# Optimization experiments

Measured on AMD Instinct MI355X. Metric: run time of the kernel, lower is better.

Reference implementation:

```python
import jax, jax.numpy as jnp
import numpy as np

I = 256   # input_size
H = 512   # hidden_size
B = 8192  # batch


def setup_inputs() -> dict:
    key = jax.random.key(0)
    ks = jax.random.split(key, 16)
    def rn(k, shape, scale):
        return (jax.random.normal(k, shape, dtype=jnp.float32) * scale)
    inp = {
        "x": rn(ks[0], (B, I), 1.0),
        "h": rn(ks[1], (B, H), 0.1),
        "c": rn(ks[2], (B, H), 0.1),
        # attention MLP: Linear(I+H -> I), Linear(I -> I)
        "aw0": rn(ks[3], (I, I + H), (I + H) ** -0.5),
        "ab0": rn(ks[4], (I,), 0.01),
        "aw1": rn(ks[5], (I, I), I ** -0.5),
        "ab1": rn(ks[6], (I,), 0.01),
        # LSTMCell params, PyTorch layout: [4H, I] / [4H, H], gate order i,f,g,o
        "w_ih": rn(ks[7], (4 * H, I), I ** -0.5),
        "b_ih": rn(ks[8], (4 * H,), 0.01),
        "w_hh": rn(ks[9], (4 * H, H), H ** -0.5),
        "b_hh": rn(ks[10], (4 * H,), 0.01),
        # output head: Linear(H -> H), Linear(H -> 1)
        "ow0": rn(ks[11], (H, H), H ** -0.5),
        "ob0": rn(ks[12], (H,), 0.01),
        "ow1": rn(ks[13], (1, H), H ** -0.5),
        "ob1": rn(ks[14], (1,), 0.01),
    }
    return inp


def reference(x, h, c, aw0, ab0, aw1, ab1, w_ih, b_ih, w_hh, b_hh, ow0, ob0, ow1, ob1):
    # attention gate over the input features
    xh = jnp.concatenate([x, h], axis=1)                    # [B, I+H]
    a0 = jax.nn.relu(xh @ aw0.T + ab0)                      # [B, I]
    logits = a0 @ aw1.T + ab1                               # [B, I]
    attn = jax.nn.softmax(logits, axis=1)                   # attention == 1
    x_att = x * attn                                        # [B, I]

    # LSTMCell (torch gate order: i, f, g, o)
    gates = x_att @ w_ih.T + b_ih + h @ w_hh.T + b_hh       # [B, 4H]
    i_g, f_g, g_g, o_g = jnp.split(gates, 4, axis=1)
    i_g = jax.nn.sigmoid(i_g)
    f_g = jax.nn.sigmoid(f_g)
    g_g = jnp.tanh(g_g)
    o_g = jax.nn.sigmoid(o_g)
    c_new = f_g * c + i_g * g_g
    h_new = o_g * jnp.tanh(c_new)

    # 2-layer MLP head -> sigmoid scalar per row
    out = jax.nn.relu(h_new @ ow0.T + ob0)                  # [B, H]
    out = jax.nn.sigmoid(out @ ow1.T + ob1)                 # [B, 1]
    return (out, h_new, c_new, attn)
```

## Files before the change

### kernel.cpp

```cpp
#include <hip/hip_runtime.h>
#include <hip/hip_bf16.h>

#define BROWS 8192
#define IDIM 256
#define HDIM 512
#define KCAT 768
#define G4 2048

typedef __bf16 bf16_t;
typedef bf16_t bf16x8 __attribute__((ext_vector_type(8)));
typedef float f32x4 __attribute__((ext_vector_type(4)));

__device__ __forceinline__ f32x4 mfma16(bf16x8 a, bf16x8 b, f32x4 c) {
    return __builtin_amdgcn_mfma_f32_16x16x32_bf16(a, b, c, 0, 0, 0);
}

__device__ __forceinline__ ushort f2bf(float f) {
    union { float f; unsigned u; } v; v.f = f;
    unsigned u = v.u;
    unsigned r = (u + 0x7fffu + ((u >> 16) & 1u)) >> 16;
    return (ushort)r;
}

__device__ __forceinline__ float bf2f(ushort u) {
    union { unsigned u; float f; } v; v.u = (unsigned)u << 16; return v.f;
}

__device__ __forceinline__ float sigmoidf_(float x) {
    return 1.f / (1.f + __expf(-x));
}
__device__ __forceinline__ float tanhf_(float x) {
    return 1.f - 2.f / (__expf(2.f * x) + 1.f);
}

typedef __attribute__((address_space(1))) const unsigned gas_u32;
typedef __attribute__((address_space(3))) unsigned las_u32;
__device__ __forceinline__ void gld_lds16(const void* g, void* l) {
    __builtin_amdgcn_global_load_lds((gas_u32*)g, (las_u32*)l, 16, 0, 0);
}

__global__ void __launch_bounds__(256) prep_kernel(
        const float* __restrict__ x, const float* __restrict__ h,
        const float* __restrict__ aw0, const float* __restrict__ aw1,
        const float* __restrict__ w_ih, const float* __restrict__ w_hh,
        const float* __restrict__ ow0,
        ushort* __restrict__ xh, ushort* __restrict__ baw0,
        ushort* __restrict__ baw1, ushort* __restrict__ wcat,
        ushort* __restrict__ bow0) {
    int idx = (blockIdx.x * 256 + threadIdx.x) * 4;
    const int N_XH = BROWS * KCAT;
    const int N_AW0 = IDIM * KCAT;
    const int N_AW1 = IDIM * IDIM;
    const int N_WCAT = G4 * KCAT;
    const int N_OW0 = HDIM * HDIM;
    float4 v;
    ushort* dst;
    if (idx < N_XH) {
        int b = idx / KCAT, k = idx - b * KCAT;
        v = (k < IDIM) ? *(const float4*)&x[b * IDIM + k]
                       : *(const float4*)&h[b * HDIM + (k - IDIM)];
        dst = &xh[idx];
    } else if ((idx -= N_XH) < N_AW0) {
        v = *(const float4*)&aw0[idx]; dst = &baw0[idx];
    } else if ((idx -= N_AW0) < N_AW1) {
        v = *(const float4*)&aw1[idx]; dst = &baw1[idx];
    } else if ((idx -= N_AW1) < N_WCAT) {
        int o = idx / KCAT, k = idx - o * KCAT;
        v = (k < IDIM) ? *(const float4*)&w_ih[o * IDIM + k]
                       : *(const float4*)&w_hh[o * HDIM + (k - IDIM)];
        dst = &wcat[idx];
    } else if ((idx -= N_WCAT) < N_OW0) {
        v = *(const float4*)&ow0[idx]; dst = &bow0[idx];
    } else {
        return;
    }
    ushort4 o4 = { f2bf(v.x), f2bf(v.y), f2bf(v.z), f2bf(v.w) };
    *(ushort4*)dst = o4;
}

template<int RELU_BF16, int NFRAG>
__global__ void __launch_bounds__(256) staged_gemm(
        const ushort* __restrict__ A, const ushort* __restrict__ W,
        const float* __restrict__ bias, void* __restrict__ outp,
        int Kdim, int out_ld) {
    __shared__ ushort As[2][4096];
    __shared__ ushort Ws[2][NFRAG * 1024];
    const int tid = threadIdx.x;
    const int lane = tid & 63, wave = tid >> 6;
    const int wm = wave >> 1, wn = wave & 1;
    const int r = lane & 15, g = lane >> 4;
    const int rb = blockIdx.x & 63, cb = blockIdx.x >> 6;
    const int row0 = rb * 128, col0 = cb * (NFRAG * 32);
    const int s_row = tid >> 2;
    const int s_sw = ((tid & 3) ^ ((s_row >> 1) & 3)) * 8;

    const ushort* aBase = A + (size_t)(row0 + s_row) * Kdim + s_sw;
    const ushort* wBase = W + (size_t)(col0 + s_row) * Kdim + s_sw;
    const int step64 = 64 * Kdim;
    const int rsw = (g ^ ((r >> 1) & 3)) * 8;

    f32x4 acc[4][NFRAG] = {};

    auto stage = [&](int buf, int t) {
        const int o = t * 32;
        gld_lds16(aBase + o,          &As[buf][wave * 512]);
        gld_lds16(aBase + o + step64, &As[buf][2048 + wave * 512]);
        gld_lds16(wBase + o,          &Ws[buf][wave * 512]);
        if (NFRAG == 4)
            gld_lds16(wBase + o + step64, &Ws[buf][2048 + wave * 512]);
    };
    auto compute = [&](int buf) {
        bf16x8 af[4], wf[NFRAG];
#pragma unroll
        for (int t = 0; t < 4; t++)
            af[t] = *(const bf16x8*)&As[buf][(wm * 4 + t) * 512 + r * 32 + rsw];
#pragma unroll
        for (int t = 0; t < NFRAG; t++)
            wf[t] = *(const bf16x8*)&Ws[buf][(wn * NFRAG + t) * 512 + r * 32 + rsw];
#pragma unroll
        for (int m = 0; m < 4; m++)
#pragma unroll
            for (int n = 0; n < NFRAG; n++)
                acc[m][n] = mfma16(af[m], wf[n], acc[m][n]);
    };

    stage(0, 0);
    const int NT = Kdim >> 5;
    int cur = 0;
    for (int t = 0; t < NT; t++) {
        __builtin_amdgcn_s_barrier();
        if (t + 1 < NT) {
            stage(cur ^ 1, t + 1);
            if (NFRAG == 4) asm volatile("s_waitcnt vmcnt(4)" ::: "memory");
            else            asm volatile("s_waitcnt vmcnt(3)" ::: "memory");
        } else {
            asm volatile("s_waitcnt vmcnt(0)" ::: "memory");
        }
        __builtin_amdgcn_s_barrier();
        compute(cur);
        cur ^= 1;
    }

#pragma unroll
    for (int n = 0; n < NFRAG; n++) {
        int col = col0 + wn * (NFRAG * 16) + n * 16 + r;
        float bv = bias[col];
#pragma unroll
        for (int m = 0; m < 4; m++) {
            int rbase = row0 + wm * 64 + m * 16 + g * 4;
#pragma unroll
            for (int reg = 0; reg < 4; reg++) {
                float v = acc[m][n][reg] + bv;
                if (RELU_BF16) {
                    v = v > 0.f ? v : 0.f;
                    ((ushort*)outp)[(size_t)(rbase + reg) * out_ld + col] = f2bf(v);
                } else {
                    ((float*)outp)[(size_t)(rbase + reg) * out_ld + col] = v;
                }
            }
        }
    }
}

__global__ void __launch_bounds__(256) attn_softmax(
        const float* __restrict__ logits, const float* __restrict__ x,
        float* __restrict__ attn_out, ushort* __restrict__ xh) {
    const int wave = threadIdx.x >> 6, lane = threadIdx.x & 63;
    const int row = blockIdx.x * 4 + wave;
    float v[4];
    float m = -1e30f;
#pragma unroll
    for (int i = 0; i < 4; i++) {
        v[i] = logits[row * IDIM + i * 64 + lane];
        m = fmaxf(m, v[i]);
    }
#pragma unroll
    for (int s = 32; s; s >>= 1) m = fmaxf(m, __shfl_xor(m, s, 64));
    float sum = 0.f;
#pragma unroll
    for (int i = 0; i < 4; i++) { v[i] = __expf(v[i] - m); sum += v[i]; }
#pragma unroll
    for (int s = 32; s; s >>= 1) sum += __shfl_xor(sum, s, 64);
    float inv = 1.f / sum;
#pragma unroll
    for (int i = 0; i < 4; i++) {
        int idx = i * 64 + lane;
        float a = v[i] * inv;
        attn_out[row * IDIM + idx] = a;
        xh[row * KCAT + idx] = f2bf(x[row * IDIM + idx] * a);
    }
}

__global__ void __launch_bounds__(1024, 4) gates_staged(
        const ushort* __restrict__ A, const ushort* __restrict__ W,
        const float* __restrict__ b_ih, const float* __restrict__ b_hh,
        const float* __restrict__ c_in,
        float* __restrict__ h_out, float* __restrict__ c_out,
        ushort* __restrict__ h_bf) {
    __shared__ ushort As[2 * 8192];
    __shared__ ushort Ws[2 * 8192];
    const int tid = threadIdx.x;
    const int lane = tid & 63, wave = tid >> 6;
    const int wm = wave >> 2, wn = wave & 3;
    const int r = lane & 15, g = lane >> 4;
    const int bid = blockIdx.x;
    const int xcd = bid & 7, local = bid >> 3;
    const int rb = xcd * 4 + (local & 3);
    const int cb = local >> 2;
    const int row0 = rb * 256;
    const int j0 = cb * 64;
    const int rl = lane >> 2, chq = lane & 3;
    const int s_sw = (chq ^ ((rl >> 1) & 3)) * 8;
    const int rsw = (g ^ ((r >> 1) & 3)) * 8;

    auto wrow = [&](int cc) {
        return ((cc >> 4) & 3) * HDIM + j0 + (cc & 15) + ((cc >> 6) << 4);
    };
    const ushort* aP = A + (size_t)(row0 + wave * 16 + rl) * KCAT + s_sw;
    const ushort* wP = W + (size_t)wrow(wave * 16 + rl) * KCAT + s_sw;

    f32x4 acc[4][4] = {};

    auto stage = [&](int buf, int t) {
        const int o = t * 32;
        gld_lds16(aP + o, &As[buf * 8192 + wave * 512]);
        gld_lds16(wP + o, &Ws[buf * 8192 + wave * 512]);
    };
    auto compute = [&](int buf) {
        bf16x8 af[4], wf[4];
#pragma unroll
        for (int m = 0; m < 4; m++)
            af[m] = *(const bf16x8*)&As[buf * 8192 + (wm * 4 + m) * 512 + r * 32 + rsw];
#pragma unroll
        for (int n = 0; n < 4; n++)
            wf[n] = *(const bf16x8*)&Ws[buf * 8192 + (wn * 4 + n) * 512 + r * 32 + rsw];
#pragma unroll
        for (int m = 0; m < 4; m++)
#pragma unroll
            for (int n = 0; n < 4; n++)
                acc[m][n] = mfma16(af[m], wf[n], acc[m][n]);
    };

    stage(0, 0);
    const int NT = KCAT >> 5;
    int cur = 0;
    for (int t = 0; t < NT; t++) {
        __builtin_amdgcn_s_barrier();
        if (t + 1 < NT) {
            stage(cur ^ 1, t + 1);
            asm volatile("s_waitcnt vmcnt(2)" ::: "memory");
        } else {
            asm volatile("s_waitcnt vmcnt(0)" ::: "memory");
        }
        __builtin_amdgcn_s_barrier();
        compute(cur);
        cur ^= 1;
    }

    const int j = j0 + wn * 16 + r;
    float bb[4];
#pragma unroll
    for (int n = 0; n < 4; n++) bb[n] = b_ih[n * HDIM + j] + b_hh[n * HDIM + j];
#pragma unroll
    for (int m = 0; m < 4; m++) {
        int rbase = row0 + wm * 64 + m * 16 + g * 4;
#pragma unroll
        for (int reg = 0; reg < 4; reg++) {
            int row = rbase + reg;
            float ig = sigmoidf_(acc[m][0][reg] + bb[0]);
            float fg = sigmoidf_(acc[m][1][reg] + bb[1]);
            float gg = tanhf_(acc[m][2][reg] + bb[2]);
            float og = sigmoidf_(acc[m][3][reg] + bb[3]);
            float cn = fg * c_in[(size_t)row * HDIM + j] + ig * gg;
            float hn = og * tanhf_(cn);
            c_out[(size_t)row * HDIM + j] = cn;
            h_out[(size_t)row * HDIM + j] = hn;
            h_bf[(size_t)row * HDIM + j] = f2bf(hn);
        }
    }
}

__global__ void __launch_bounds__(256) head_gemv(
        const ushort* __restrict__ Hrelu, const float* __restrict__ ow1,
        const float* __restrict__ ob1, float* __restrict__ outp) {
    const int wave = threadIdx.x >> 6, lane = threadIdx.x & 63;
    const int row = blockIdx.x * 4 + wave;
    typedef ushort u16x8 __attribute__((ext_vector_type(8)));
    u16x8 hv = *(const u16x8*)&Hrelu[(size_t)row * HDIM + lane * 8];
    float4 w0 = *(const float4*)&ow1[lane * 8];
    float4 w1 = *(const float4*)&ow1[lane * 8 + 4];
    float s = bf2f(hv[0]) * w0.x + bf2f(hv[1]) * w0.y + bf2f(hv[2]) * w0.z +
              bf2f(hv[3]) * w0.w + bf2f(hv[4]) * w1.x + bf2f(hv[5]) * w1.y +
              bf2f(hv[6]) * w1.z + bf2f(hv[7]) * w1.w;
#pragma unroll
    for (int sh = 32; sh; sh >>= 1) s += __shfl_xor(s, sh, 64);
    if (lane == 0) outp[row] = 1.f / (1.f + __expf(-(s + ob1[0])));
}

extern "C" void kernel_launch(void* const* d_in, const int* in_sizes, int n_in,
                              void* d_out, int out_size, void* d_ws, size_t ws_size,
                              hipStream_t stream) {
    const float* x    = (const float*)d_in[0];
    const float* h    = (const float*)d_in[1];
    const float* c    = (const float*)d_in[2];
    const float* aw0  = (const float*)d_in[3];
    const float* ab0  = (const float*)d_in[4];
    const float* aw1  = (const float*)d_in[5];
    const float* ab1  = (const float*)d_in[6];
    const float* w_ih = (const float*)d_in[7];
    const float* b_ih = (const float*)d_in[8];
    const float* w_hh = (const float*)d_in[9];
    const float* b_hh = (const float*)d_in[10];
    const float* ow0  = (const float*)d_in[11];
    const float* ob0  = (const float*)d_in[12];
    const float* ow1  = (const float*)d_in[13];
    const float* ob1  = (const float*)d_in[14];

    char* ws = (char*)d_ws;
    ushort* xh     = (ushort*)(ws + 0);
    ushort* a0     = (ushort*)(ws + 12582912);
    float*  logits = (float*) (ws + 16777216);
    ushort* hrelu  = (ushort*)(ws + 16777216);
    ushort* hbf    = (ushort*)(ws + 25165824);
    ushort* baw0   = (ushort*)(ws + 33554432);
    ushort* baw1   = (ushort*)(ws + 33947648);
    ushort* wcat   = (ushort*)(ws + 34078720);
    ushort* bow0   = (ushort*)(ws + 37224448);

    float* outv    = (float*)d_out;
    float* h_out   = outv + 8192;
    float* c_out   = outv + 4202496;
    float* attn_o  = outv + 8396800;

    prep_kernel<<<8192, 256, 0, stream>>>(x, h, aw0, aw1, w_ih, w_hh, ow0,
                                          xh, baw0, baw1, wcat, bow0);
    staged_gemm<1, 2><<<256, 256, 0, stream>>>(xh, baw0, ab0, a0, KCAT, IDIM);
    staged_gemm<0, 2><<<256, 256, 0, stream>>>(a0, baw1, ab1, logits, IDIM, IDIM);
    attn_softmax<<<2048, 256, 0, stream>>>(logits, x, attn_o, xh);
    gates_staged<<<256, 1024, 0, stream>>>(xh, wcat, b_ih, b_hh, c,
                                           h_out, c_out, hbf);
    staged_gemm<1, 4><<<256, 256, 0, stream>>>(hbf, bow0, ob0, hrelu, HDIM, HDIM);
    head_gemv<<<2048, 256, 0, stream>>>(hrelu, ow1, ob1, outv);
}
```

Before: 91.72 us.

## Retile staged GEMM to 512 threads with 2x2 fragments per wave

Rewrites the staged GEMM so each block runs 8 waves instead of 4. Each wave now owns a 2x2 grid of 16x16 MFMA tiles over a 128x64 output tile, where before it owned 4x2 or 4x4. Only the first four waves load weight tiles, and the output-head GEMM now uses 512 blocks of 64-column tiles. The aim is more waves in flight per CU and more grid parallelism to hide latency. The cost is less register-level reuse of each fragment and more LDS reads per MFMA.

```diff
diff --git a/kernel.cpp b/kernel.cpp
--- a/kernel.cpp
+++ b/kernel.cpp
@@ -78,49 +78,46 @@
     *(ushort4*)dst = o4;
 }
 
-template<int RELU_BF16, int NFRAG>
-__global__ void __launch_bounds__(256) staged_gemm(
+template<int RELU_BF16>
+__global__ void __launch_bounds__(512, 4) staged_gemm(
         const ushort* __restrict__ A, const ushort* __restrict__ W,
         const float* __restrict__ bias, void* __restrict__ outp,
         int Kdim, int out_ld) {
     __shared__ ushort As[2][4096];
-    __shared__ ushort Ws[2][NFRAG * 1024];
+    __shared__ ushort Ws[2][2048];
     const int tid = threadIdx.x;
     const int lane = tid & 63, wave = tid >> 6;
     const int wm = wave >> 1, wn = wave & 1;
     const int r = lane & 15, g = lane >> 4;
     const int rb = blockIdx.x & 63, cb = blockIdx.x >> 6;
-    const int row0 = rb * 128, col0 = cb * (NFRAG * 32);
-    const int s_row = tid >> 2;
-    const int s_sw = ((tid & 3) ^ ((s_row >> 1) & 3)) * 8;
-
-    const ushort* aBase = A + (size_t)(row0 + s_row) * Kdim + s_sw;
-    const ushort* wBase = W + (size_t)(col0 + s_row) * Kdim + s_sw;
-    const int step64 = 64 * Kdim;
+    const int row0 = rb * 128, col0 = cb * 64;
+    const int rl = lane >> 2, chq = lane & 3;
+    const int s_sw = (chq ^ ((rl >> 1) & 3)) * 8;
     const int rsw = (g ^ ((r >> 1) & 3)) * 8;
-
-    f32x4 acc[4][NFRAG] = {};
+    const bool doW = wave < 4;
+
+    const ushort* aP = A + (size_t)(row0 + wave * 16 + rl) * Kdim + s_sw;
+    const ushort* wP = W + (size_t)(col0 + (wave & 3) * 16 + rl) * Kdim + s_sw;
+
+    f32x4 acc[2][2] = {};
 
     auto stage = [&](int buf, int t) {
         const int o = t * 32;
-        gld_lds16(aBase + o,          &As[buf][wave * 512]);
-        gld_lds16(aBase + o + step64, &As[buf][2048 + wave * 512]);
-        gld_lds16(wBase + o,          &Ws[buf][wave * 512]);
-        if (NFRAG == 4)
-            gld_lds16(wBase + o + step64, &Ws[buf][2048 + wave * 512]);
+        gld_lds16(aP + o, &As[buf][wave * 512]);
+        if (doW) gld_lds16(wP + o, &Ws[buf][(wave & 3) * 512]);
     };
     auto compute = [&](int buf) {
-        bf16x8 af[4], wf[NFRAG];
-#pragma unroll
-        for (int t = 0; t < 4; t++)
-            af[t] = *(const bf16x8*)&As[buf][(wm * 4 + t) * 512 + r * 32 + rsw];
-#pragma unroll
-        for (int t = 0; t < NFRAG; t++)
-            wf[t] = *(const bf16x8*)&Ws[buf][(wn * NFRAG + t) * 512 + r * 32 + rsw];
-#pragma unroll
-        for (int m = 0; m < 4; m++)
-#pragma unroll
-            for (int n = 0; n < NFRAG; n++)
+        bf16x8 af[2], wf[2];
+#pragma unroll
+        for (int m = 0; m < 2; m++)
+            af[m] = *(const bf16x8*)&As[buf][(wm * 2 + m) * 512 + r * 32 + rsw];
+#pragma unroll
+        for (int n = 0; n < 2; n++)
+            wf[n] = *(const bf16x8*)&Ws[buf][(wn * 2 + n) * 512 + r * 32 + rsw];
+#pragma unroll
+        for (int m = 0; m < 2; m++)
+#pragma unroll
+            for (int n = 0; n < 2; n++)
                 acc[m][n] = mfma16(af[m], wf[n], acc[m][n]);
     };
 
@@ -131,8 +128,8 @@
         __builtin_amdgcn_s_barrier();
         if (t + 1 < NT) {
             stage(cur ^ 1, t + 1);
-            if (NFRAG == 4) asm volatile("s_waitcnt vmcnt(4)" ::: "memory");
-            else            asm volatile("s_waitcnt vmcnt(3)" ::: "memory");
+            if (doW) asm volatile("s_waitcnt vmcnt(2)" ::: "memory");
+            else     asm volatile("s_waitcnt vmcnt(1)" ::: "memory");
         } else {
             asm volatile("s_waitcnt vmcnt(0)" ::: "memory");
         }
@@ -142,12 +139,12 @@
     }
 
 #pragma unroll
-    for (int n = 0; n < NFRAG; n++) {
-        int col = col0 + wn * (NFRAG * 16) + n * 16 + r;
+    for (int n = 0; n < 2; n++) {
+        int col = col0 + wn * 32 + n * 16 + r;
         float bv = bias[col];
 #pragma unroll
-        for (int m = 0; m < 4; m++) {
-            int rbase = row0 + wm * 64 + m * 16 + g * 4;
+        for (int m = 0; m < 2; m++) {
+            int rbase = row0 + wm * 32 + m * 16 + g * 4;
 #pragma unroll
             for (int reg = 0; reg < 4; reg++) {
                 float v = acc[m][n][reg] + bv;
@@ -334,11 +331,11 @@
 
     prep_kernel<<<8192, 256, 0, stream>>>(x, h, aw0, aw1, w_ih, w_hh, ow0,
                                           xh, baw0, baw1, wcat, bow0);
-    staged_gemm<1, 2><<<256, 256, 0, stream>>>(xh, baw0, ab0, a0, KCAT, IDIM);
-    staged_gemm<0, 2><<<256, 256, 0, stream>>>(a0, baw1, ab1, logits, IDIM, IDIM);
+    staged_gemm<1><<<256, 512, 0, stream>>>(xh, baw0, ab0, a0, KCAT, IDIM);
+    staged_gemm<0><<<256, 512, 0, stream>>>(a0, baw1, ab1, logits, IDIM, IDIM);
     attn_softmax<<<2048, 256, 0, stream>>>(logits, x, attn_o, xh);
     gates_staged<<<256, 1024, 0, stream>>>(xh, wcat, b_ih, b_hh, c,
                                            h_out, c_out, hbf);
-    staged_gemm<1, 4><<<256, 256, 0, stream>>>(hbf, bow0, ob0, hrelu, HDIM, HDIM);
+    staged_gemm<1><<<512, 512, 0, stream>>>(hbf, bow0, ob0, hrelu, HDIM, HDIM);
     head_gemv<<<2048, 256, 0, stream>>>(hrelu, ow1, ob1, outv);
 }
```

Measured after the change: 89.12 us. 1.03x faster.
